# Performance work log

Measured on AMD Instinct MI355X. Metric: run time of the kernel, lower is better.

## Reference

```python
import jax, jax.numpy as jnp
import numpy as np

N = 50000
E = 800000
NODE_SIZE = 64
NUM_RADIAL = 20
CUTOFF = 5.0


def setup_inputs() -> dict:
    key = jax.random.key(0)
    ks = jax.random.split(key, 12)
    node_scalar = jax.random.normal(ks[0], (N, NODE_SIZE), dtype=jnp.float32)
    node_vector = jax.random.normal(ks[1], (N, 3, NODE_SIZE), dtype=jnp.float32)
    edge = jax.random.randint(ks[2], (E, 2), 0, N, dtype=jnp.int64)
    edge_diff = jax.random.normal(ks[3], (E, 3), dtype=jnp.float32)
    # positive distances in (0, cutoff]; most edges inside cutoff
    edge_dist = jax.random.uniform(ks[4], (E, 1), dtype=jnp.float32) * CUTOFF + 1e-2
    s = 1.0 / np.sqrt(NODE_SIZE)
    r = 1.0 / np.sqrt(NUM_RADIAL)
    W1 = jax.random.normal(ks[5], (NODE_SIZE, NODE_SIZE), dtype=jnp.float32) * s
    b1 = jnp.zeros((NODE_SIZE,), dtype=jnp.float32)
    W2 = jax.random.normal(ks[6], (NODE_SIZE, 3 * NODE_SIZE), dtype=jnp.float32) * s
    b2 = jnp.zeros((3 * NODE_SIZE,), dtype=jnp.float32)
    Wf = jax.random.normal(ks[7], (NUM_RADIAL, 3 * NODE_SIZE), dtype=jnp.float32) * r
    bf = jnp.zeros((3 * NODE_SIZE,), dtype=jnp.float32)
    return {"node_scalar": node_scalar, "node_vector": node_vector, "edge": edge,
            "edge_diff": edge_diff, "edge_dist": edge_dist,
            "W1": W1, "b1": b1, "W2": W2, "b2": b2, "Wf": Wf, "bf": bf}


def reference(node_scalar, node_vector, edge, edge_diff, edge_dist, W1, b1, W2, b2, Wf, bf):
    S = NODE_SIZE
    n_nodes = node_scalar.shape[0]
    # sinc radial basis: sin(n*pi*d/cutoff)/d, n=1..num_radial -> [E, R]
    n = jnp.arange(1, NUM_RADIAL + 1, dtype=edge_dist.dtype)
    rbf = jnp.sin(edge_dist * n * jnp.pi / CUTOFF) / edge_dist
    filter_weight = rbf @ Wf + bf                       # [E, 3S]
    # cosine cutoff, broadcast [E,1] over [E,3S]
    cut = jnp.where(edge_dist < CUTOFF,
                    0.5 * (jnp.cos(jnp.pi * edge_dist / CUTOFF) + 1.0),
                    jnp.zeros((), edge_dist.dtype))
    filter_weight = filter_weight * cut
    # scalar message MLP on nodes: Linear -> SiLU -> Linear
    scalar_out = jax.nn.silu(node_scalar @ W1 + b1) @ W2 + b2   # [N, 3S]
    src = edge[:, 1]
    dst = edge[:, 0]
    filter_out = filter_weight * scalar_out[src]        # [E, 3S]
    gate_state_vector = filter_out[:, :S]
    gate_edge_vector = filter_out[:, S:2 * S]
    message_scalar = filter_out[:, 2 * S:]
    unit = (edge_diff / edge_dist)[:, :, None]          # [E, 3, 1]
    message_vector = node_vector[src] * gate_state_vector[:, None, :] + gate_edge_vector[:, None, :] * unit  # [E,3,S]
    residual_scalar = jax.ops.segment_sum(message_scalar, dst, num_segments=n_nodes)
    residual_vector = jax.ops.segment_sum(message_vector, dst, num_segments=n_nodes)
    return node_scalar + residual_scalar, node_vector + residual_vector
```

## Files before the change

### kernel.cpp

```cpp
#include <hip/hip_runtime.h>
#include <hip/hip_bf16.h>
#include <math.h>

#define N_NODES 50000
#define N_EDGES 800000
#define NRAD 20
#define NBLK 196
#define CAP 48
#define NGRP 64
#define GSZ 782
#define MLPB 782

typedef short bf16x8 __attribute__((ext_vector_type(8)));
typedef _Float16 f16x8 __attribute__((ext_vector_type(8)));
typedef float f32x4 __attribute__((ext_vector_type(4)));
typedef int i32x4 __attribute__((ext_vector_type(4)));
typedef int i32x2 __attribute__((ext_vector_type(2)));

__device__ __forceinline__ unsigned short f2b(float f) {
    union { __hip_bfloat16 h; unsigned short u; } cv;
    cv.h = __float2bfloat16(f);
    return cv.u;
}
__device__ __forceinline__ unsigned int packh2(float a, float b) {
    union { _Float16 h; unsigned short u; } A, B;
    A.h = (_Float16)a; B.h = (_Float16)b;
    return (unsigned int)A.u | ((unsigned int)B.u << 16);
}
__device__ __forceinline__ f32x4 mfma16(bf16x8 a, bf16x8 b, f32x4 c) {
    return __builtin_amdgcn_mfma_f32_16x16x32_bf16(a, b, c, 0, 0, 0);
}
__device__ __forceinline__ f32x4 mfma16h(f16x8 a, f16x8 b, f32x4 c) {
    return __builtin_amdgcn_mfma_f32_16x16x32_f16(a, b, c, 0, 0, 0);
}
__device__ __forceinline__ f32x4 mkv4(float x, float y, float z, float w) {
    f32x4 v; v[0] = x; v[1] = y; v[2] = z; v[3] = w; return v;
}
union afu { i32x4 i; f16x8 h; };

__global__ __launch_bounds__(256) void prep0_kernel(
    int* __restrict__ counts, int* __restrict__ qctr,
    const float* __restrict__ W1, const float* __restrict__ W2, const float* __restrict__ Wf,
    const float* __restrict__ bfv,
    unsigned short* __restrict__ W1t, unsigned short* __restrict__ W2t,
    unsigned int* __restrict__ Bfp) {
    int i = blockIdx.x * 256 + threadIdx.x;
    if (i < N_NODES) counts[i] = 0;
    if (i < NGRP * 32) qctr[i] = 0;
    if (i < 192 * 64) {
        int n = i >> 6, k = i & 63;
        W2t[i] = f2b(W2[k * 192 + n]);
        if (i < 64 * 64) W1t[i] = f2b(W1[k * 64 + n]);
        if (i < 768) {
            int cblk = i >> 6, l = i & 63;
            int cp = cblk * 16 + (l & 15);
            int kb = (l >> 4) * 8;
            unsigned d[4];
#pragma unroll
            for (int w = 0; w < 4; w++) {
                int k0 = kb + 2 * w, k1 = k0 + 1;
                float B0 = (k0 < 20) ? Wf[k0 * 192 + cp] : ((k0 == 20) ? bfv[cp] : 0.0f);
                float B1 = (k1 < 20) ? Wf[k1 * 192 + cp] : ((k1 == 20) ? bfv[cp] : 0.0f);
                d[w] = packh2(B0, B1);
            }
            Bfp[i * 4 + 0] = d[0];
            Bfp[i * 4 + 1] = d[1];
            Bfp[i * 4 + 2] = d[2];
            Bfp[i * 4 + 3] = d[3];
        }
    }
}

__global__ void hist_kernel(const int2* __restrict__ edge2, int* __restrict__ counts) {
    int e = blockIdx.x * blockDim.x + threadIdx.x;
    if (e < N_EDGES) atomicAdd(&counts[edge2[e].x], 1);
}

__global__ __launch_bounds__(256) void scanall_kernel(const int* __restrict__ counts,
                                                      int* __restrict__ offs,
                                                      int* __restrict__ cursors) {
    __shared__ int ss[256];
    int t = threadIdx.x, b = blockIdx.x;
    int lim = b * 256;
    int s = 0;
    for (int i = t; i < lim; i += 256) s += counts[i];
    ss[t] = s;
    __syncthreads();
    for (int k = 128; k > 0; k >>= 1) {
        if (t < k) ss[t] += ss[t + k];
        __syncthreads();
    }
    int base0 = ss[0];
    __syncthreads();
    int i = lim + t;
    int v = (i < N_NODES) ? counts[i] : 0;
    ss[t] = v;
    __syncthreads();
    for (int off = 1; off < 256; off <<= 1) {
        int u = (t >= off) ? ss[t - off] : 0;
        __syncthreads();
        ss[t] += u;
        __syncthreads();
    }
    int excl = base0 + ss[t] - v;
    if (i < N_NODES) {
        offs[i] = excl;
        cursors[i] = excl;
    }
    if (i == N_NODES - 1) offs[N_NODES] = excl + v;
}

template <int C>
__device__ __forceinline__ void bucket_body(
    int e, const int2* __restrict__ edge2, const float* __restrict__ ediff,
    const float* __restrict__ edist, int* __restrict__ cursors,
    f32x4* __restrict__ pack) {
    if (e >= N_EDGES) return;
    i32x2 edv = __builtin_nontemporal_load((const i32x2*)&edge2[e]);
    int dst = edv[0];
    int src = edv[1];
    int slot = atomicAdd(&cursors[dst], 1);
    size_t pos;
    if (C > 0) {
        if (slot >= C) return;
        pos = (size_t)dst * C + slot;
    } else {
        pos = (size_t)slot;
    }
    float dist = __builtin_nontemporal_load(&edist[e]);
    float d0 = __builtin_nontemporal_load(&ediff[3 * e]);
    float d1 = __builtin_nontemporal_load(&ediff[3 * e + 1]);
    float d2 = __builtin_nontemporal_load(&ediff[3 * e + 2]);
    float inv = __builtin_amdgcn_rcpf(dist);
    f32x4* P = pack + pos * 2;
    P[0] = mkv4(__int_as_float(src), d0 * inv, d1 * inv, d2 * inv);
    P[1] = mkv4(dist, inv, 0.0f, 0.0f);
}

__device__ __forceinline__ void mlp_body(
    int bid, int t, const float* __restrict__ ns, const float* __restrict__ nv,
    const unsigned short* __restrict__ W1t, const float* __restrict__ b1,
    const unsigned short* __restrict__ W2t, const float* __restrict__ b2,
    unsigned short* __restrict__ snb) {
    __shared__ unsigned short LB[64 * 200];
    unsigned short* H = LB;
    unsigned short* O = LB;
    int lane = t & 63;
    int w = t >> 6;
    int c15 = lane & 15;
    int quad = lane >> 4;
    int base = bid * 64;

    int node = base + 16 * w + c15;
    if (node >= N_NODES) node = N_NODES - 1;

    bf16x8 a0, a1;
    {
        const float* xr = ns + (size_t)node * 64 + quad * 8;
        float4 p0 = *(const float4*)xr;
        float4 p1 = *(const float4*)(xr + 4);
        float4 p2 = *(const float4*)(xr + 32);
        float4 p3 = *(const float4*)(xr + 36);
        a0[0] = (short)f2b(p0.x); a0[1] = (short)f2b(p0.y);
        a0[2] = (short)f2b(p0.z); a0[3] = (short)f2b(p0.w);
        a0[4] = (short)f2b(p1.x); a0[5] = (short)f2b(p1.y);
        a0[6] = (short)f2b(p1.z); a0[7] = (short)f2b(p1.w);
        a1[0] = (short)f2b(p2.x); a1[1] = (short)f2b(p2.y);
        a1[2] = (short)f2b(p2.z); a1[3] = (short)f2b(p2.w);
        a1[4] = (short)f2b(p3.x); a1[5] = (short)f2b(p3.y);
        a1[6] = (short)f2b(p3.z); a1[7] = (short)f2b(p3.w);
    }

#pragma unroll
    for (int nt = 0; nt < 4; nt++) {
        float bc = b1[nt * 16 + c15];
        f32x4 acc = {bc, bc, bc, bc};
        bf16x8 w0 = *(const bf16x8*)(W1t + (nt * 16 + c15) * 64 + quad * 8);
        bf16x8 w1 = *(const bf16x8*)(W1t + (nt * 16 + c15) * 64 + 32 + quad * 8);
        acc = mfma16(a0, w0, acc);
        acc = mfma16(a1, w1, acc);
#pragma unroll
        for (int r = 0; r < 4; r++) {
            float v = acc[r];
            v = v / (1.0f + __expf(-v));
            H[(16 * w + quad * 4 + r) * 72 + nt * 16 + c15] = f2b(v);
        }
    }

    bf16x8 h0 = *(const bf16x8*)(H + (16 * w + c15) * 72 + quad * 8);
    bf16x8 h1 = *(const bf16x8*)(H + (16 * w + c15) * 72 + 32 + quad * 8);
    __syncthreads();

#pragma unroll
    for (int nt = 0; nt < 12; nt++) {
        float bc = b2[nt * 16 + c15];
        f32x4 acc = {bc, bc, bc, bc};
        bf16x8 w0 = *(const bf16x8*)(W2t + (nt * 16 + c15) * 64 + quad * 8);
        bf16x8 w1 = *(const bf16x8*)(W2t + (nt * 16 + c15) * 64 + 32 + quad * 8);
        acc = mfma16(h0, w0, acc);
        acc = mfma16(h1, w1, acc);
#pragma unroll
        for (int r = 0; r < 4; r++)
            O[(16 * w + quad * 4 + r) * 200 + nt * 16 + c15] = f2b(acc[r]);
    }
    __syncthreads();

    int nb = min(64, N_NODES - base);
    for (int idx = t; idx < nb * 64; idx += 256) {
        int row = idx >> 6, ll = idx & 63;
        unsigned short o0 = O[row * 200 + ll];
        unsigned short o1 = O[row * 200 + 64 + ll];
        unsigned short o2 = O[row * 200 + 128 + ll];
        int nd = base + row;
        float v0 = nv[(size_t)nd * 192 + ll];
        float v1 = nv[(size_t)nd * 192 + 64 + ll];
        float v2 = nv[(size_t)nd * 192 + 128 + ll];
        uint3 pkv;
        pkv.x = (unsigned int)o0 | ((unsigned int)o1 << 16);
        pkv.y = (unsigned int)o2 | ((unsigned int)f2b(v0) << 16);
        pkv.z = (unsigned int)f2b(v1) | ((unsigned int)f2b(v2) << 16);
        *(uint3*)((char*)snb + (size_t)nd * 768 + ll * 12) = pkv;
    }
}

template <int C>
__global__ __launch_bounds__(256) void work_kernel(
    const float* __restrict__ ns, const float* __restrict__ nv,
    const unsigned short* __restrict__ W1t, const float* __restrict__ b1,
    const unsigned short* __restrict__ W2t, const float* __restrict__ b2,
    unsigned short* __restrict__ snb,
    const int2* __restrict__ edge2, const float* __restrict__ ediff,
    const float* __restrict__ edist, int* __restrict__ cursors,
    f32x4* __restrict__ pack) {
    int bid = blockIdx.x;
    if (bid < MLPB) {
        mlp_body(bid, threadIdx.x, ns, nv, W1t, b1, W2t, b2, snb);
    } else {
        int e = (bid - MLPB) * 256 + threadIdx.x;
        bucket_body<C>(e, edge2, ediff, edist, cursors, pack);
    }
}

template <int C>
__global__ __launch_bounds__(256) void gather_kernel(
    const float* __restrict__ ns, const float* __restrict__ nv,
    const unsigned int* __restrict__ Bfp,
    const unsigned short* __restrict__ snb, const int* __restrict__ offs,
    const f32x4* __restrict__ pack, float* __restrict__ out0, float* __restrict__ out1,
    int* __restrict__ qctr) {
    __shared__ char LSH[2048 + 12288];
    int t = threadIdx.x;
    int l = t & 63;
    int w = t >> 6;
    int c = l & 15;
    int quad = l >> 4;
    char* slab = LSH + w * 512;
    i32x4* BfL = (i32x4*)(LSH + 2048);

    for (int j = t; j < 768; j += 256) BfL[j] = ((const i32x4*)Bfp)[j];
    __syncthreads();

    const char* packb = (const char*)pack;
    const char* snbb = (const char*)snb;

    int grp = __builtin_amdgcn_readfirstlane((int)(blockIdx.x & (NGRP - 1)));
    int gbase = grp * GSZ;
    int glim = min(gbase + GSZ, N_NODES);
    int* ctr = qctr + grp * 32;

    int tk = 0;
    if (l == 0) tk = atomicAdd(ctr, 1);
    int n = gbase + __builtin_amdgcn_readfirstlane(tk);

    while (n < glim) {
        if (l == 0) tk = atomicAdd(ctr, 1);

        int start, end;
        if (C > 0) {
            start = n * C;
            int cc = __builtin_amdgcn_readfirstlane(offs[n]);
            if (cc > C) cc = C;
            end = start + cc;
        } else {
            start = __builtin_amdgcn_readfirstlane(offs[n]);
            end = __builtin_amdgcn_readfirstlane(offs[n + 1]);
        }

        float accs[4] = {0.f, 0.f, 0.f, 0.f};
        float A0[4] = {0.f, 0.f, 0.f, 0.f};
        float A1[4] = {0.f, 0.f, 0.f, 0.f};
        float A2[4] = {0.f, 0.f, 0.f, 0.f};

        for (int cb = start; cb < end; cb += 16) {
            int cnt_t = end - cb; if (cnt_t > 16) cnt_t = 16;
            int vb = cnt_t * 32;
            if (l < 32) {
                i32x4 sv = {0, 0, 0, 0};
                if (l * 16 < vb)
                    sv = __builtin_nontemporal_load(
                        (const i32x4*)(packb + (size_t)(unsigned)cb * 32 + (size_t)(l * 16)));
                *(i32x4*)(slab + l * 16) = sv;
            }
            afu au;
            {
                i32x2 di = *(const i32x2*)(slab + c * 32 + 16);
                float dist = __int_as_float(di[0]);
                float inv = __int_as_float(di[1]);
                float x = dist * 0.62831853071795864769f;
                float s1 = __sinf(x);
                float c1 = __cosf(x);
                float cut = (dist > 0.0f && dist < 5.0f) ? 0.5f * (c1 + 1.0f) : 0.0f;
                float ic = inv * cut;
                float t2 = 2.0f * c1;
                float r[NRAD];
                float sn = s1, sp = 0.0f;
#pragma unroll
                for (int k = 0; k < NRAD; k++) {
                    r[k] = sn * ic;
                    float nx = t2 * sn - sp;
                    sp = sn;
                    sn = nx;
                }
                unsigned pw[11];
#pragma unroll
                for (int j = 0; j < 10; j++) pw[j] = packh2(r[2 * j], r[2 * j + 1]);
                pw[10] = packh2(cut, 0.0f);
                au.i[0] = (int)(quad == 0 ? pw[0] : quad == 1 ? pw[4] : quad == 2 ? pw[8] : 0u);
                au.i[1] = (int)(quad == 0 ? pw[1] : quad == 1 ? pw[5] : quad == 2 ? pw[9] : 0u);
                au.i[2] = (int)(quad == 0 ? pw[2] : quad == 1 ? pw[6] : quad == 2 ? pw[10] : 0u);
                au.i[3] = (int)(quad == 0 ? pw[3] : quad == 1 ? pw[7] : 0u);
            }
            i32x4 q[4];
#pragma unroll
            for (int r = 0; r < 4; r++)
                q[r] = *(const i32x4*)(slab + (quad * 4 + r) * 32);
            uint3 G[4][4];
#pragma unroll
            for (int r = 0; r < 4; r++) {
                const char* sp = snbb + (size_t)(unsigned)q[r][0] * 768 + c * 12;
#pragma unroll
                for (int b = 0; b < 4; b++)
                    G[b][r] = *(const uint3*)(sp + b * 192);
            }
#pragma unroll
            for (int b = 0; b < 4; b++) {
                f32x4 z = {0.f, 0.f, 0.f, 0.f};
                afu b0, b4, b8;
                b0.i = BfL[b * 64 + l];
                b4.i = BfL[(b + 4) * 64 + l];
                b8.i = BfL[(b + 8) * 64 + l];
                f32x4 D0 = mfma16h(au.h, b0.h, z);
                f32x4 D4 = mfma16h(au.h, b4.h, z);
                f32x4 D8 = mfma16h(au.h, b8.h, z);
#pragma unroll
                for (int r = 0; r < 4; r++) {
                    uint3 g = G[b][r];
                    float u0 = __int_as_float(q[r][1]);
                    float u1 = __int_as_float(q[r][2]);
                    float u2 = __int_as_float(q[r][3]);
                    float s0 = __uint_as_float(g.x << 16);
                    float s1 = __uint_as_float(g.x & 0xffff0000u);
                    float s2 = __uint_as_float(g.y << 16);
                    float v0 = __uint_as_float(g.y & 0xffff0000u);
                    float v1 = __uint_as_float(g.z << 16);
                    float v2 = __uint_as_float(g.z & 0xffff0000u);
                    float gg0 = D0[r] * s0;
                    float gg1 = D4[r] * s1;
                    accs[b] = fmaf(D8[r], s2, accs[b]);
                    A0[b] = fmaf(v0, gg0, fmaf(u0, gg1, A0[b]));
                    A1[b] = fmaf(v1, gg0, fmaf(u1, gg1, A1[b]));
                    A2[b] = fmaf(v2, gg0, fmaf(u2, gg1, A2[b]));
                }
            }
        }

#pragma unroll
        for (int b = 0; b < 4; b++) {
            accs[b] += __shfl_xor(accs[b], 16); accs[b] += __shfl_xor(accs[b], 32);
            A0[b] += __shfl_xor(A0[b], 16);     A0[b] += __shfl_xor(A0[b], 32);
            A1[b] += __shfl_xor(A1[b], 16);     A1[b] += __shfl_xor(A1[b], 32);
            A2[b] += __shfl_xor(A2[b], 16);     A2[b] += __shfl_xor(A2[b], 32);
        }
        float rs = quad == 0 ? accs[0] : quad == 1 ? accs[1] : quad == 2 ? accs[2] : accs[3];
        float r0 = quad == 0 ? A0[0] : quad == 1 ? A0[1] : quad == 2 ? A0[2] : A0[3];
        float r1 = quad == 0 ? A1[0] : quad == 1 ? A1[1] : quad == 2 ? A1[2] : A1[3];
        float r2 = quad == 0 ? A2[0] : quad == 1 ? A2[1] : quad == 2 ? A2[2] : A2[3];

        size_t b64 = (size_t)n * 64 + l, b192 = (size_t)n * 192 + l;
        __builtin_nontemporal_store(
            __builtin_nontemporal_load(ns + b64) + rs, out0 + b64);
        __builtin_nontemporal_store(
            __builtin_nontemporal_load(nv + b192) + r0, out1 + b192);
        __builtin_nontemporal_store(
            __builtin_nontemporal_load(nv + b192 + 64) + r1, out1 + b192 + 64);
        __builtin_nontemporal_store(
            __builtin_nontemporal_load(nv + b192 + 128) + r2, out1 + b192 + 128);

        n = gbase + __builtin_amdgcn_readfirstlane(tk);
    }
}

extern "C" void kernel_launch(void* const* d_in, const int* in_sizes, int n_in,
                              void* d_out, int out_size, void* d_ws, size_t ws_size,
                              hipStream_t stream) {
    const float* ns    = (const float*)d_in[0];
    const float* nv    = (const float*)d_in[1];
    const int2*  edge2 = (const int2*)d_in[2];
    const float* ediff = (const float*)d_in[3];
    const float* edist = (const float*)d_in[4];
    const float* W1    = (const float*)d_in[5];
    const float* b1    = (const float*)d_in[6];
    const float* W2    = (const float*)d_in[7];
    const float* b2    = (const float*)d_in[8];
    const float* Wf    = (const float*)d_in[9];
    const float* bfv   = (const float*)d_in[10];

    float* out0 = (float*)d_out;
    float* out1 = out0 + (size_t)N_NODES * 64;

    const size_t cap_pack = (size_t)N_NODES * CAP * 32;
    const size_t need_cap = cap_pack + (size_t)N_NODES * 768 + 8192 + 24576 + 12288 +
                            (size_t)N_NODES * 4 + 4096 + NGRP * 32 * 4;
    bool capmode = ws_size >= need_cap;

    char* wsp = (char*)d_ws;
    f32x4* pack = (f32x4*)wsp;
    wsp += capmode ? cap_pack : (size_t)N_EDGES * 32;
    unsigned short* snb = (unsigned short*)wsp;     wsp += (size_t)N_NODES * 768;
    unsigned short* W1t = (unsigned short*)wsp;     wsp += 64 * 64 * 2;
    unsigned short* W2t = (unsigned short*)wsp;     wsp += 192 * 64 * 2;
    unsigned int* Bfp = (unsigned int*)wsp;         wsp += 12288;
    int* counts  = (int*)wsp;
    int* offs    = counts + N_NODES;
    int* cursors = offs + (N_NODES + 1);
    int* qctr = capmode ? (counts + N_NODES) : (cursors + N_NODES);

    const int BUCB = (N_EDGES + 255) / 256;

    if (capmode) {
        prep0_kernel<<<NBLK, 256, 0, stream>>>(counts, qctr, W1, W2, Wf, bfv,
                                               W1t, W2t, Bfp);
        work_kernel<CAP><<<MLPB + BUCB, 256, 0, stream>>>(
            ns, nv, W1t, b1, W2t, b2, snb, edge2, ediff, edist, counts, pack);
        gather_kernel<CAP><<<2048, 256, 0, stream>>>(ns, nv, Bfp, snb, counts, pack,
                                                     out0, out1, qctr);
    } else {
        prep0_kernel<<<NBLK, 256, 0, stream>>>(counts, qctr, W1, W2, Wf, bfv,
                                               W1t, W2t, Bfp);
        hist_kernel<<<BUCB, 256, 0, stream>>>(edge2, counts);
        scanall_kernel<<<NBLK, 256, 0, stream>>>(counts, offs, cursors);
        work_kernel<0><<<MLPB + BUCB, 256, 0, stream>>>(
            ns, nv, W1t, b1, W2t, b2, snb, edge2, ediff, edist, cursors, pack);
        gather_kernel<0><<<2048, 256, 0, stream>>>(ns, nv, Bfp, snb, offs, pack,
                                                   out0, out1, qctr);
    }
}
```

Before: 265.3 us.

## Fuse prep, MLP/bucket and gather stages into one cooperative persistent kernel

Replaces the three kernel launches in capacity mode with a single cooperative kernel that runs prep, then MLP and edge bucketing, then gather, separated by grid-wide syncs. The grid is sized from the occupancy query and capped at 1280 blocks, and the MLP and bucket work items are looped over persistently. The aim is to remove launch gaps and kernel-boundary drains between stages. In exchange it adds grid.sync overhead and caps occupancy through launch bounds and shared memory sized for the largest stage, and it falls back to the old three-kernel path if the cooperative launch fails.

```diff
diff --git a/kernel.cpp b/kernel.cpp
--- a/kernel.cpp
+++ b/kernel.cpp
@@ -1,6 +1,9 @@
 #include <hip/hip_runtime.h>
+#include <hip/hip_cooperative_groups.h>
 #include <hip/hip_bf16.h>
 #include <math.h>
+
+namespace cg = cooperative_groups;
 
 #define N_NODES 50000
 #define N_EDGES 800000
@@ -10,6 +13,7 @@
 #define NGRP 64
 #define GSZ 782
 #define MLPB 782
+#define BUCB 3125
 
 typedef short bf16x8 __attribute__((ext_vector_type(8)));
 typedef _Float16 f16x8 __attribute__((ext_vector_type(8)));
@@ -38,13 +42,13 @@
 }
 union afu { i32x4 i; f16x8 h; };
 
-__global__ __launch_bounds__(256) void prep0_kernel(
-    int* __restrict__ counts, int* __restrict__ qctr,
-    const float* __restrict__ W1, const float* __restrict__ W2, const float* __restrict__ Wf,
-    const float* __restrict__ bfv,
+
+__device__ __forceinline__ void prep_body(
+    int i, int* __restrict__ counts, int* __restrict__ qctr,
+    const float* __restrict__ W1, const float* __restrict__ W2,
+    const float* __restrict__ Wf, const float* __restrict__ bfv,
     unsigned short* __restrict__ W1t, unsigned short* __restrict__ W2t,
     unsigned int* __restrict__ Bfp) {
-    int i = blockIdx.x * 256 + threadIdx.x;
     if (i < N_NODES) counts[i] = 0;
     if (i < NGRP * 32) qctr[i] = 0;
     if (i < 192 * 64) {
@@ -69,45 +73,6 @@
             Bfp[i * 4 + 3] = d[3];
         }
     }
-}
-
-__global__ void hist_kernel(const int2* __restrict__ edge2, int* __restrict__ counts) {
-    int e = blockIdx.x * blockDim.x + threadIdx.x;
-    if (e < N_EDGES) atomicAdd(&counts[edge2[e].x], 1);
-}
-
-__global__ __launch_bounds__(256) void scanall_kernel(const int* __restrict__ counts,
-                                                      int* __restrict__ offs,
-                                                      int* __restrict__ cursors) {
-    __shared__ int ss[256];
-    int t = threadIdx.x, b = blockIdx.x;
-    int lim = b * 256;
-    int s = 0;
-    for (int i = t; i < lim; i += 256) s += counts[i];
-    ss[t] = s;
-    __syncthreads();
-    for (int k = 128; k > 0; k >>= 1) {
-        if (t < k) ss[t] += ss[t + k];
-        __syncthreads();
-    }
-    int base0 = ss[0];
-    __syncthreads();
-    int i = lim + t;
-    int v = (i < N_NODES) ? counts[i] : 0;
-    ss[t] = v;
-    __syncthreads();
-    for (int off = 1; off < 256; off <<= 1) {
-        int u = (t >= off) ? ss[t - off] : 0;
-        __syncthreads();
-        ss[t] += u;
-        __syncthreads();
-    }
-    int excl = base0 + ss[t] - v;
-    if (i < N_NODES) {
-        offs[i] = excl;
-        cursors[i] = excl;
-    }
-    if (i == N_NODES - 1) offs[N_NODES] = excl + v;
 }
 
 template <int C>
@@ -141,8 +106,7 @@
     int bid, int t, const float* __restrict__ ns, const float* __restrict__ nv,
     const unsigned short* __restrict__ W1t, const float* __restrict__ b1,
     const unsigned short* __restrict__ W2t, const float* __restrict__ b2,
-    unsigned short* __restrict__ snb) {
-    __shared__ unsigned short LB[64 * 200];
+    unsigned short* __restrict__ snb, unsigned short* __restrict__ LB) {
     unsigned short* H = LB;
     unsigned short* O = LB;
     int lane = t & 63;
@@ -224,38 +188,18 @@
 }
 
 template <int C>
-__global__ __launch_bounds__(256) void work_kernel(
+__device__ __forceinline__ void gather_body(
+    int bid, int t, char* __restrict__ SMEM,
     const float* __restrict__ ns, const float* __restrict__ nv,
-    const unsigned short* __restrict__ W1t, const float* __restrict__ b1,
-    const unsigned short* __restrict__ W2t, const float* __restrict__ b2,
-    unsigned short* __restrict__ snb,
-    const int2* __restrict__ edge2, const float* __restrict__ ediff,
-    const float* __restrict__ edist, int* __restrict__ cursors,
-    f32x4* __restrict__ pack) {
-    int bid = blockIdx.x;
-    if (bid < MLPB) {
-        mlp_body(bid, threadIdx.x, ns, nv, W1t, b1, W2t, b2, snb);
-    } else {
-        int e = (bid - MLPB) * 256 + threadIdx.x;
-        bucket_body<C>(e, edge2, ediff, edist, cursors, pack);
-    }
-}
-
-template <int C>
-__global__ __launch_bounds__(256) void gather_kernel(
-    const float* __restrict__ ns, const float* __restrict__ nv,
-    const unsigned int* __restrict__ Bfp,
-    const unsigned short* __restrict__ snb, const int* __restrict__ offs,
-    const f32x4* __restrict__ pack, float* __restrict__ out0, float* __restrict__ out1,
-    int* __restrict__ qctr) {
-    __shared__ char LSH[2048 + 12288];
-    int t = threadIdx.x;
+    const unsigned int* __restrict__ Bfp, const unsigned short* __restrict__ snb,
+    const int* __restrict__ offs, const f32x4* __restrict__ pack,
+    float* __restrict__ out0, float* __restrict__ out1, int* __restrict__ qctr) {
     int l = t & 63;
     int w = t >> 6;
     int c = l & 15;
     int quad = l >> 4;
-    char* slab = LSH + w * 512;
-    i32x4* BfL = (i32x4*)(LSH + 2048);
+    char* slab = SMEM + w * 512;
+    i32x4* BfL = (i32x4*)(SMEM + 2048);
 
     for (int j = t; j < 768; j += 256) BfL[j] = ((const i32x4*)Bfp)[j];
     __syncthreads();
@@ -263,7 +207,7 @@
     const char* packb = (const char*)pack;
     const char* snbb = (const char*)snb;
 
-    int grp = __builtin_amdgcn_readfirstlane((int)(blockIdx.x & (NGRP - 1)));
+    int grp = __builtin_amdgcn_readfirstlane(bid & (NGRP - 1));
     int gbase = grp * GSZ;
     int glim = min(gbase + GSZ, N_NODES);
     int* ctr = qctr + grp * 32;
@@ -400,6 +344,121 @@
     }
 }
 
+template <int C>
+__global__ __launch_bounds__(256, 5) void fused_kernel(
+    const float* __restrict__ ns, const float* __restrict__ nv,
+    const int2* __restrict__ edge2, const float* __restrict__ ediff,
+    const float* __restrict__ edist,
+    const float* __restrict__ W1, const float* __restrict__ b1,
+    const float* __restrict__ W2, const float* __restrict__ b2,
+    const float* __restrict__ Wf, const float* __restrict__ bfv,
+    unsigned short* __restrict__ W1t, unsigned short* __restrict__ W2t,
+    unsigned int* __restrict__ Bfp, int* __restrict__ counts,
+    int* __restrict__ qctr, f32x4* __restrict__ pack,
+    unsigned short* __restrict__ snb,
+    float* __restrict__ out0, float* __restrict__ out1) {
+    __shared__ char SMEM[25600];
+    cg::grid_group grid = cg::this_grid();
+    int t = threadIdx.x;
+    int bid = blockIdx.x;
+    int nb = gridDim.x;
+
+    prep_body(bid * 256 + t, counts, qctr, W1, W2, Wf, bfv, W1t, W2t, Bfp);
+    grid.sync();
+
+    for (int u = bid; u < MLPB + BUCB; u += nb) {
+        if (u < MLPB) {
+            mlp_body(u, t, ns, nv, W1t, b1, W2t, b2, snb, (unsigned short*)SMEM);
+        } else {
+            bucket_body<C>((u - MLPB) * 256 + t, edge2, ediff, edist, counts, pack);
+        }
+        __syncthreads();
+    }
+    grid.sync();
+
+    gather_body<C>(bid, t, SMEM, ns, nv, Bfp, snb, counts, pack, out0, out1, qctr);
+}
+
+__global__ __launch_bounds__(256) void prep0_kernel(
+    int* __restrict__ counts, int* __restrict__ qctr,
+    const float* __restrict__ W1, const float* __restrict__ W2,
+    const float* __restrict__ Wf, const float* __restrict__ bfv,
+    unsigned short* __restrict__ W1t, unsigned short* __restrict__ W2t,
+    unsigned int* __restrict__ Bfp) {
+    prep_body(blockIdx.x * 256 + threadIdx.x, counts, qctr, W1, W2, Wf, bfv,
+              W1t, W2t, Bfp);
+}
+
+__global__ void hist_kernel(const int2* __restrict__ edge2, int* __restrict__ counts) {
+    int e = blockIdx.x * blockDim.x + threadIdx.x;
+    if (e < N_EDGES) atomicAdd(&counts[edge2[e].x], 1);
+}
+
+__global__ __launch_bounds__(256) void scanall_kernel(const int* __restrict__ counts,
+                                                      int* __restrict__ offs,
+                                                      int* __restrict__ cursors) {
+    __shared__ int ss[256];
+    int t = threadIdx.x, b = blockIdx.x;
+    int lim = b * 256;
+    int s = 0;
+    for (int i = t; i < lim; i += 256) s += counts[i];
+    ss[t] = s;
+    __syncthreads();
+    for (int k = 128; k > 0; k >>= 1) {
+        if (t < k) ss[t] += ss[t + k];
+        __syncthreads();
+    }
+    int base0 = ss[0];
+    __syncthreads();
+    int i = lim + t;
+    int v = (i < N_NODES) ? counts[i] : 0;
+    ss[t] = v;
+    __syncthreads();
+    for (int off = 1; off < 256; off <<= 1) {
+        int u = (t >= off) ? ss[t - off] : 0;
+        __syncthreads();
+        ss[t] += u;
+        __syncthreads();
+    }
+    int excl = base0 + ss[t] - v;
+    if (i < N_NODES) {
+        offs[i] = excl;
+        cursors[i] = excl;
+    }
+    if (i == N_NODES - 1) offs[N_NODES] = excl + v;
+}
+
+template <int C>
+__global__ __launch_bounds__(256) void work_kernel(
+    const float* __restrict__ ns, const float* __restrict__ nv,
+    const unsigned short* __restrict__ W1t, const float* __restrict__ b1,
+    const unsigned short* __restrict__ W2t, const float* __restrict__ b2,
+    unsigned short* __restrict__ snb,
+    const int2* __restrict__ edge2, const float* __restrict__ ediff,
+    const float* __restrict__ edist, int* __restrict__ cursors,
+    f32x4* __restrict__ pack) {
+    __shared__ char SMEM[25600];
+    int bid = blockIdx.x;
+    if (bid < MLPB) {
+        mlp_body(bid, threadIdx.x, ns, nv, W1t, b1, W2t, b2, snb,
+                 (unsigned short*)SMEM);
+    } else {
+        bucket_body<C>((bid - MLPB) * 256 + threadIdx.x, edge2, ediff, edist,
+                       cursors, pack);
+    }
+}
+
+template <int C>
+__global__ __launch_bounds__(256) void gather_kernel(
+    const float* __restrict__ ns, const float* __restrict__ nv,
+    const unsigned int* __restrict__ Bfp, const unsigned short* __restrict__ snb,
+    const int* __restrict__ offs, const f32x4* __restrict__ pack,
+    float* __restrict__ out0, float* __restrict__ out1, int* __restrict__ qctr) {
+    __shared__ char SMEM[14336];
+    gather_body<C>(blockIdx.x, threadIdx.x, SMEM, ns, nv, Bfp, snb,
+                   offs, pack, out0, out1, qctr);
+}
+
 extern "C" void kernel_launch(void* const* d_in, const int* in_sizes, int n_in,
                               void* d_out, int out_size, void* d_ws, size_t ws_size,
                               hipStream_t stream) {
@@ -435,15 +494,32 @@
     int* cursors = offs + (N_NODES + 1);
     int* qctr = capmode ? (counts + N_NODES) : (cursors + N_NODES);
 
-    const int BUCB = (N_EDGES + 255) / 256;
-
     if (capmode) {
-        prep0_kernel<<<NBLK, 256, 0, stream>>>(counts, qctr, W1, W2, Wf, bfv,
-                                               W1t, W2t, Bfp);
-        work_kernel<CAP><<<MLPB + BUCB, 256, 0, stream>>>(
-            ns, nv, W1t, b1, W2t, b2, snb, edge2, ediff, edist, counts, pack);
-        gather_kernel<CAP><<<2048, 256, 0, stream>>>(ns, nv, Bfp, snb, counts, pack,
-                                                     out0, out1, qctr);
+        int maxb = 0;
+        hipError_t oe = hipOccupancyMaxActiveBlocksPerMultiprocessor(
+            &maxb, fused_kernel<CAP>, 256, 0);
+        int grid = (oe == hipSuccess && maxb > 0) ? maxb * 256 : 0;
+        if (grid > 1280) grid = 1280;
+        grid &= ~(NGRP - 1);
+        bool coop_ok = grid >= 256;
+        if (coop_ok) {
+            void* args[] = {
+                (void*)&ns, (void*)&nv, (void*)&edge2, (void*)&ediff, (void*)&edist,
+                (void*)&W1, (void*)&b1, (void*)&W2, (void*)&b2, (void*)&Wf,
+                (void*)&bfv, (void*)&W1t, (void*)&W2t, (void*)&Bfp, (void*)&counts,
+                (void*)&qctr, (void*)&pack, (void*)&snb, (void*)&out0, (void*)&out1};
+            hipError_t le = hipLaunchCooperativeKernel(
+                fused_kernel<CAP>, dim3(grid), dim3(256), args, 0, stream);
+            if (le != hipSuccess) coop_ok = false;
+        }
+        if (!coop_ok) {
+            prep0_kernel<<<NBLK, 256, 0, stream>>>(counts, qctr, W1, W2, Wf, bfv,
+                                                   W1t, W2t, Bfp);
+            work_kernel<CAP><<<MLPB + BUCB, 256, 0, stream>>>(
+                ns, nv, W1t, b1, W2t, b2, snb, edge2, ediff, edist, counts, pack);
+            gather_kernel<CAP><<<2048, 256, 0, stream>>>(ns, nv, Bfp, snb, counts,
+                                                         pack, out0, out1, qctr);
+        }
     } else {
         prep0_kernel<<<NBLK, 256, 0, stream>>>(counts, qctr, W1, W2, Wf, bfv,
                                                W1t, W2t, Bfp);
```

Result: slower. 679.1 us (+156.0%).

## Bucket edge indices only and gather edge attributes in the gather kernel

Applied to the files above, without the earlier changes.

The bucketing pass now writes only a 4-byte edge index per slot instead of a 32-byte packed record holding src, unit vector, dist and inverse dist. The gather kernel reads the index, then does random-access loads of edge, edist and ediff to rebuild the unit vector and src in LDS, staging 48 edges per chunk. The goal is to cut write and read traffic for the intermediate pack buffer. The cost is scattered, uncoalesced reads of the original edge arrays inside the gather loop, plus extra LDS use.

```diff
diff --git a/kernel.cpp b/kernel.cpp
--- a/kernel.cpp
+++ b/kernel.cpp
@@ -10,6 +10,7 @@
 #define NGRP 64
 #define GSZ 782
 #define MLPB 782
+#define BUCB 3125
 
 typedef short bf16x8 __attribute__((ext_vector_type(8)));
 typedef _Float16 f16x8 __attribute__((ext_vector_type(8)));
@@ -33,15 +34,12 @@
 __device__ __forceinline__ f32x4 mfma16h(f16x8 a, f16x8 b, f32x4 c) {
     return __builtin_amdgcn_mfma_f32_16x16x32_f16(a, b, c, 0, 0, 0);
 }
-__device__ __forceinline__ f32x4 mkv4(float x, float y, float z, float w) {
-    f32x4 v; v[0] = x; v[1] = y; v[2] = z; v[3] = w; return v;
-}
 union afu { i32x4 i; f16x8 h; };
 
 __global__ __launch_bounds__(256) void prep0_kernel(
     int* __restrict__ counts, int* __restrict__ qctr,
-    const float* __restrict__ W1, const float* __restrict__ W2, const float* __restrict__ Wf,
-    const float* __restrict__ bfv,
+    const float* __restrict__ W1, const float* __restrict__ W2,
+    const float* __restrict__ Wf, const float* __restrict__ bfv,
     unsigned short* __restrict__ W1t, unsigned short* __restrict__ W2t,
     unsigned int* __restrict__ Bfp) {
     int i = blockIdx.x * 256 + threadIdx.x;
@@ -112,13 +110,11 @@
 
 template <int C>
 __device__ __forceinline__ void bucket_body(
-    int e, const int2* __restrict__ edge2, const float* __restrict__ ediff,
-    const float* __restrict__ edist, int* __restrict__ cursors,
-    f32x4* __restrict__ pack) {
+    int e, const int2* __restrict__ edge2, int* __restrict__ cursors,
+    int* __restrict__ eidx) {
     if (e >= N_EDGES) return;
     i32x2 edv = __builtin_nontemporal_load((const i32x2*)&edge2[e]);
     int dst = edv[0];
-    int src = edv[1];
     int slot = atomicAdd(&cursors[dst], 1);
     size_t pos;
     if (C > 0) {
@@ -127,22 +123,14 @@
     } else {
         pos = (size_t)slot;
     }
-    float dist = __builtin_nontemporal_load(&edist[e]);
-    float d0 = __builtin_nontemporal_load(&ediff[3 * e]);
-    float d1 = __builtin_nontemporal_load(&ediff[3 * e + 1]);
-    float d2 = __builtin_nontemporal_load(&ediff[3 * e + 2]);
-    float inv = __builtin_amdgcn_rcpf(dist);
-    f32x4* P = pack + pos * 2;
-    P[0] = mkv4(__int_as_float(src), d0 * inv, d1 * inv, d2 * inv);
-    P[1] = mkv4(dist, inv, 0.0f, 0.0f);
+    eidx[pos] = e;
 }
 
 __device__ __forceinline__ void mlp_body(
     int bid, int t, const float* __restrict__ ns, const float* __restrict__ nv,
     const unsigned short* __restrict__ W1t, const float* __restrict__ b1,
     const unsigned short* __restrict__ W2t, const float* __restrict__ b2,
-    unsigned short* __restrict__ snb) {
-    __shared__ unsigned short LB[64 * 200];
+    unsigned short* __restrict__ snb, unsigned short* __restrict__ LB) {
     unsigned short* H = LB;
     unsigned short* O = LB;
     int lane = t & 63;
@@ -229,38 +217,38 @@
     const unsigned short* __restrict__ W1t, const float* __restrict__ b1,
     const unsigned short* __restrict__ W2t, const float* __restrict__ b2,
     unsigned short* __restrict__ snb,
-    const int2* __restrict__ edge2, const float* __restrict__ ediff,
-    const float* __restrict__ edist, int* __restrict__ cursors,
-    f32x4* __restrict__ pack) {
+    const int2* __restrict__ edge2, int* __restrict__ cursors,
+    int* __restrict__ eidx) {
+    __shared__ char SMEM[25600];
     int bid = blockIdx.x;
     if (bid < MLPB) {
-        mlp_body(bid, threadIdx.x, ns, nv, W1t, b1, W2t, b2, snb);
+        mlp_body(bid, threadIdx.x, ns, nv, W1t, b1, W2t, b2, snb,
+                 (unsigned short*)SMEM);
     } else {
-        int e = (bid - MLPB) * 256 + threadIdx.x;
-        bucket_body<C>(e, edge2, ediff, edist, cursors, pack);
+        bucket_body<C>((bid - MLPB) * 256 + threadIdx.x, edge2, cursors, eidx);
     }
 }
 
 template <int C>
 __global__ __launch_bounds__(256) void gather_kernel(
     const float* __restrict__ ns, const float* __restrict__ nv,
-    const unsigned int* __restrict__ Bfp,
-    const unsigned short* __restrict__ snb, const int* __restrict__ offs,
-    const f32x4* __restrict__ pack, float* __restrict__ out0, float* __restrict__ out1,
-    int* __restrict__ qctr) {
-    __shared__ char LSH[2048 + 12288];
+    const unsigned int* __restrict__ Bfp, const unsigned short* __restrict__ snb,
+    const int* __restrict__ offs, const int* __restrict__ eidx,
+    const int2* __restrict__ edge2, const float* __restrict__ ediff,
+    const float* __restrict__ edist,
+    float* __restrict__ out0, float* __restrict__ out1, int* __restrict__ qctr) {
+    __shared__ char SMEM[4096 + 12288];
     int t = threadIdx.x;
     int l = t & 63;
     int w = t >> 6;
     int c = l & 15;
     int quad = l >> 4;
-    char* slab = LSH + w * 512;
-    i32x4* BfL = (i32x4*)(LSH + 2048);
+    char* slab = SMEM + w * 1024;
+    i32x4* BfL = (i32x4*)(SMEM + 4096);
 
     for (int j = t; j < 768; j += 256) BfL[j] = ((const i32x4*)Bfp)[j];
     __syncthreads();
 
-    const char* packb = (const char*)pack;
     const char* snbb = (const char*)snb;
 
     int grp = __builtin_amdgcn_readfirstlane((int)(blockIdx.x & (NGRP - 1)));
@@ -278,9 +266,9 @@
         int start, end;
         if (C > 0) {
             start = n * C;
-            int cc = __builtin_amdgcn_readfirstlane(offs[n]);
-            if (cc > C) cc = C;
-            end = start + cc;
+            int cc0 = __builtin_amdgcn_readfirstlane(offs[n]);
+            if (cc0 > C) cc0 = C;
+            end = start + cc0;
         } else {
             start = __builtin_amdgcn_readfirstlane(offs[n]);
             end = __builtin_amdgcn_readfirstlane(offs[n + 1]);
@@ -291,85 +279,101 @@
         float A1[4] = {0.f, 0.f, 0.f, 0.f};
         float A2[4] = {0.f, 0.f, 0.f, 0.f};
 
-        for (int cb = start; cb < end; cb += 16) {
-            int cnt_t = end - cb; if (cnt_t > 16) cnt_t = 16;
-            int vb = cnt_t * 32;
-            if (l < 32) {
-                i32x4 sv = {0, 0, 0, 0};
-                if (l * 16 < vb)
-                    sv = __builtin_nontemporal_load(
-                        (const i32x4*)(packb + (size_t)(unsigned)cb * 32 + (size_t)(l * 16)));
-                *(i32x4*)(slab + l * 16) = sv;
+        for (int cb = start; cb < end; cb += 48) {
+            int cc = end - cb; if (cc > 48) cc = 48;
+            if (l < 48) {
+                int srcv = 0;
+                float u0 = 0.f, u1 = 0.f, u2 = 0.f, dv = 0.f;
+                if (l < cc) {
+                    int e = eidx[cb + l];
+                    i32x2 ed = *(const i32x2*)&edge2[e];
+                    srcv = ed[1];
+                    dv = edist[e];
+                    float inv = __builtin_amdgcn_rcpf(dv);
+                    u0 = ediff[3 * e] * inv;
+                    u1 = ediff[3 * e + 1] * inv;
+                    u2 = ediff[3 * e + 2] * inv;
+                }
+                i32x4 qv;
+                qv[0] = srcv;
+                qv[1] = __float_as_int(u0);
+                qv[2] = __float_as_int(u1);
+                qv[3] = __float_as_int(u2);
+                *(i32x4*)(slab + l * 16) = qv;
+                *(float*)(slab + 768 + l * 4) = dv;
             }
-            afu au;
-            {
-                i32x2 di = *(const i32x2*)(slab + c * 32 + 16);
-                float dist = __int_as_float(di[0]);
-                float inv = __int_as_float(di[1]);
-                float x = dist * 0.62831853071795864769f;
-                float s1 = __sinf(x);
-                float c1 = __cosf(x);
-                float cut = (dist > 0.0f && dist < 5.0f) ? 0.5f * (c1 + 1.0f) : 0.0f;
-                float ic = inv * cut;
-                float t2 = 2.0f * c1;
-                float r[NRAD];
-                float sn = s1, sp = 0.0f;
-#pragma unroll
-                for (int k = 0; k < NRAD; k++) {
-                    r[k] = sn * ic;
-                    float nx = t2 * sn - sp;
-                    sp = sn;
-                    sn = nx;
+
+            int ntile = (cc + 15) >> 4;
+            for (int tt = 0; tt < ntile; tt++) {
+                afu au;
+                {
+                    float dist = *(const float*)(slab + 768 + (tt * 16 + c) * 4);
+                    float inv = dist > 0.0f ? __builtin_amdgcn_rcpf(dist) : 0.0f;
+                    float x = dist * 0.62831853071795864769f;
+                    float s1 = __sinf(x);
+                    float c1 = __cosf(x);
+                    float cut = (dist > 0.0f && dist < 5.0f) ? 0.5f * (c1 + 1.0f) : 0.0f;
+                    float ic = inv * cut;
+                    float t2 = 2.0f * c1;
+                    float r[NRAD];
+                    float sn = s1, sp = 0.0f;
+#pragma unroll
+                    for (int k = 0; k < NRAD; k++) {
+                        r[k] = sn * ic;
+                        float nx = t2 * sn - sp;
+                        sp = sn;
+                        sn = nx;
+                    }
+                    unsigned pw[11];
+#pragma unroll
+                    for (int j = 0; j < 10; j++) pw[j] = packh2(r[2 * j], r[2 * j + 1]);
+                    pw[10] = packh2(cut, 0.0f);
+                    au.i[0] = (int)(quad == 0 ? pw[0] : quad == 1 ? pw[4] : quad == 2 ? pw[8] : 0u);
+                    au.i[1] = (int)(quad == 0 ? pw[1] : quad == 1 ? pw[5] : quad == 2 ? pw[9] : 0u);
+                    au.i[2] = (int)(quad == 0 ? pw[2] : quad == 1 ? pw[6] : quad == 2 ? pw[10] : 0u);
+                    au.i[3] = (int)(quad == 0 ? pw[3] : quad == 1 ? pw[7] : 0u);
                 }
-                unsigned pw[11];
-#pragma unroll
-                for (int j = 0; j < 10; j++) pw[j] = packh2(r[2 * j], r[2 * j + 1]);
-                pw[10] = packh2(cut, 0.0f);
-                au.i[0] = (int)(quad == 0 ? pw[0] : quad == 1 ? pw[4] : quad == 2 ? pw[8] : 0u);
-                au.i[1] = (int)(quad == 0 ? pw[1] : quad == 1 ? pw[5] : quad == 2 ? pw[9] : 0u);
-                au.i[2] = (int)(quad == 0 ? pw[2] : quad == 1 ? pw[6] : quad == 2 ? pw[10] : 0u);
-                au.i[3] = (int)(quad == 0 ? pw[3] : quad == 1 ? pw[7] : 0u);
-            }
-            i32x4 q[4];
-#pragma unroll
-            for (int r = 0; r < 4; r++)
-                q[r] = *(const i32x4*)(slab + (quad * 4 + r) * 32);
-            uint3 G[4][4];
-#pragma unroll
-            for (int r = 0; r < 4; r++) {
-                const char* sp = snbb + (size_t)(unsigned)q[r][0] * 768 + c * 12;
-#pragma unroll
-                for (int b = 0; b < 4; b++)
-                    G[b][r] = *(const uint3*)(sp + b * 192);
-            }
-#pragma unroll
-            for (int b = 0; b < 4; b++) {
-                f32x4 z = {0.f, 0.f, 0.f, 0.f};
-                afu b0, b4, b8;
-                b0.i = BfL[b * 64 + l];
-                b4.i = BfL[(b + 4) * 64 + l];
-                b8.i = BfL[(b + 8) * 64 + l];
-                f32x4 D0 = mfma16h(au.h, b0.h, z);
-                f32x4 D4 = mfma16h(au.h, b4.h, z);
-                f32x4 D8 = mfma16h(au.h, b8.h, z);
+                i32x4 q[4];
+#pragma unroll
+                for (int r = 0; r < 4; r++)
+                    q[r] = *(const i32x4*)(slab + (tt * 16 + quad * 4 + r) * 16);
+                uint3 G[4][4];
 #pragma unroll
                 for (int r = 0; r < 4; r++) {
-                    uint3 g = G[b][r];
-                    float u0 = __int_as_float(q[r][1]);
-                    float u1 = __int_as_float(q[r][2]);
-                    float u2 = __int_as_float(q[r][3]);
-                    float s0 = __uint_as_float(g.x << 16);
-                    float s1 = __uint_as_float(g.x & 0xffff0000u);
-                    float s2 = __uint_as_float(g.y << 16);
-                    float v0 = __uint_as_float(g.y & 0xffff0000u);
-                    float v1 = __uint_as_float(g.z << 16);
-                    float v2 = __uint_as_float(g.z & 0xffff0000u);
-                    float gg0 = D0[r] * s0;
-                    float gg1 = D4[r] * s1;
-                    accs[b] = fmaf(D8[r], s2, accs[b]);
-                    A0[b] = fmaf(v0, gg0, fmaf(u0, gg1, A0[b]));
-                    A1[b] = fmaf(v1, gg0, fmaf(u1, gg1, A1[b]));
-                    A2[b] = fmaf(v2, gg0, fmaf(u2, gg1, A2[b]));
+                    const char* sp = snbb + (size_t)(unsigned)q[r][0] * 768 + c * 12;
+#pragma unroll
+                    for (int b = 0; b < 4; b++)
+                        G[b][r] = *(const uint3*)(sp + b * 192);
+                }
+#pragma unroll
+                for (int b = 0; b < 4; b++) {
+                    f32x4 z = {0.f, 0.f, 0.f, 0.f};
+                    afu b0, b4, b8;
+                    b0.i = BfL[b * 64 + l];
+                    b4.i = BfL[(b + 4) * 64 + l];
+                    b8.i = BfL[(b + 8) * 64 + l];
+                    f32x4 D0 = mfma16h(au.h, b0.h, z);
+                    f32x4 D4 = mfma16h(au.h, b4.h, z);
+                    f32x4 D8 = mfma16h(au.h, b8.h, z);
+#pragma unroll
+                    for (int r = 0; r < 4; r++) {
+                        uint3 g = G[b][r];
+                        float u0 = __int_as_float(q[r][1]);
+                        float u1 = __int_as_float(q[r][2]);
+                        float u2 = __int_as_float(q[r][3]);
+                        float s0 = __uint_as_float(g.x << 16);
+                        float s1 = __uint_as_float(g.x & 0xffff0000u);
+                        float s2 = __uint_as_float(g.y << 16);
+                        float v0 = __uint_as_float(g.y & 0xffff0000u);
+                        float v1 = __uint_as_float(g.z << 16);
+                        float v2 = __uint_as_float(g.z & 0xffff0000u);
+                        float gg0 = D0[r] * s0;
+                        float gg1 = D4[r] * s1;
+                        accs[b] = fmaf(D8[r], s2, accs[b]);
+                        A0[b] = fmaf(v0, gg0, fmaf(u0, gg1, A0[b]));
+                        A1[b] = fmaf(v1, gg0, fmaf(u1, gg1, A1[b]));
+                        A2[b] = fmaf(v2, gg0, fmaf(u2, gg1, A2[b]));
+                    }
                 }
             }
         }
@@ -418,14 +422,14 @@
     float* out0 = (float*)d_out;
     float* out1 = out0 + (size_t)N_NODES * 64;
 
-    const size_t cap_pack = (size_t)N_NODES * CAP * 32;
-    const size_t need_cap = cap_pack + (size_t)N_NODES * 768 + 8192 + 24576 + 12288 +
+    const size_t cap_eidx = (size_t)N_NODES * CAP * 4;
+    const size_t need_cap = cap_eidx + (size_t)N_NODES * 768 + 8192 + 24576 + 12288 +
                             (size_t)N_NODES * 4 + 4096 + NGRP * 32 * 4;
     bool capmode = ws_size >= need_cap;
 
     char* wsp = (char*)d_ws;
-    f32x4* pack = (f32x4*)wsp;
-    wsp += capmode ? cap_pack : (size_t)N_EDGES * 32;
+    int* eidx = (int*)wsp;
+    wsp += capmode ? cap_eidx : (size_t)N_EDGES * 4;
     unsigned short* snb = (unsigned short*)wsp;     wsp += (size_t)N_NODES * 768;
     unsigned short* W1t = (unsigned short*)wsp;     wsp += 64 * 64 * 2;
     unsigned short* W2t = (unsigned short*)wsp;     wsp += 192 * 64 * 2;
@@ -435,23 +439,21 @@
     int* cursors = offs + (N_NODES + 1);
     int* qctr = capmode ? (counts + N_NODES) : (cursors + N_NODES);
 
-    const int BUCB = (N_EDGES + 255) / 256;
-
     if (capmode) {
         prep0_kernel<<<NBLK, 256, 0, stream>>>(counts, qctr, W1, W2, Wf, bfv,
                                                W1t, W2t, Bfp);
         work_kernel<CAP><<<MLPB + BUCB, 256, 0, stream>>>(
-            ns, nv, W1t, b1, W2t, b2, snb, edge2, ediff, edist, counts, pack);
-        gather_kernel<CAP><<<2048, 256, 0, stream>>>(ns, nv, Bfp, snb, counts, pack,
-                                                     out0, out1, qctr);
+            ns, nv, W1t, b1, W2t, b2, snb, edge2, counts, eidx);
+        gather_kernel<CAP><<<2048, 256, 0, stream>>>(
+            ns, nv, Bfp, snb, counts, eidx, edge2, ediff, edist, out0, out1, qctr);
     } else {
         prep0_kernel<<<NBLK, 256, 0, stream>>>(counts, qctr, W1, W2, Wf, bfv,
                                                W1t, W2t, Bfp);
         hist_kernel<<<BUCB, 256, 0, stream>>>(edge2, counts);
         scanall_kernel<<<NBLK, 256, 0, stream>>>(counts, offs, cursors);
         work_kernel<0><<<MLPB + BUCB, 256, 0, stream>>>(
-            ns, nv, W1t, b1, W2t, b2, snb, edge2, ediff, edist, cursors, pack);
-        gather_kernel<0><<<2048, 256, 0, stream>>>(ns, nv, Bfp, snb, offs, pack,
-                                                   out0, out1, qctr);
-    }
-}
+            ns, nv, W1t, b1, W2t, b2, snb, edge2, cursors, eidx);
+        gather_kernel<0><<<2048, 256, 0, stream>>>(
+            ns, nv, Bfp, snb, offs, eidx, edge2, ediff, edist, out0, out1, qctr);
+    }
+}
```

New measurement: 303.1 us. 1.14x slower.
